# Kernel tuning notes

Hardware: AMD Instinct MI355X
Metric: run time of the kernel (lower is better)

## Reference

```python
import jax, jax.numpy as jnp
import numpy as np

# Kernel codes matching style 'L;O2;P2;Y2,1,1;R0.5;W1,1'
KERNEL_CODES = ['L', 'O', 'P', 'Y', 'R', 'W']
SM_TEMP = 1.0


def _norm_sq(q, k):
    # q: [n,l,h,e], k: [n,s,h,e] -> [n,h,l,s]
    q2 = jnp.einsum('nlhe,nlhe->nhl', q, q)[..., None]        # [n,h,l,1]
    k2 = jnp.einsum('nshe,nshe->nhs', k, k)[:, :, None, :]     # [n,h,1,s]
    qk = jnp.einsum('nlhe,nshe->nhls', q, k)
    return q2 + k2 - 2.0 * qk


def _kernel(code, q, k):
    if code == 'L':
        return jnp.einsum('nlhe,nshe->nhls', q, k)
    if code == 'O':  # -log(1 + ns^(p/2)), p=2
        return -jnp.log1p(_norm_sq(q, k))
    if code == 'P':  # -(ns)^(p/2), p=2
        return -_norm_sq(q, k)
    if code == 'Y':  # (alpha*<q,k> + c)^p, p=2, alpha=1, c=1
        d = jnp.einsum('nlhe,nshe->nhls', q, k)
        return (d + 1.0) ** 2
    if code == 'R':  # exp(-gamma*ns), gamma=0.5
        return jnp.exp(-0.5 * _norm_sq(q, k))
    if code == 'W':  # cos(ns/a)*exp(-ns/b), a=b=1
        ns = _norm_sq(q, k)
        return jnp.cos(ns) * jnp.exp(-ns)
    raise ValueError(code)


def setup_inputs() -> dict:
    key = jax.random.key(0)
    k1, k2, k3, k4 = jax.random.split(key, 4)
    N, L, S, H, E, K = 2, 1024, 1024, 8, 64, 6
    return {
        'query': jax.random.normal(k1, (N, L, H, E), dtype=jnp.float32),
        'key': jax.random.normal(k2, (N, S, H, E), dtype=jnp.float32),
        'attn_mask_add': jnp.zeros((N, L, S), dtype=jnp.float32),
        'key_lengths_add': jnp.zeros((N, S), dtype=jnp.float32),
        'M': jax.random.uniform(k3, (H, E, K), dtype=jnp.float32),
        'C': jax.random.uniform(k4, (K, H, E, E), dtype=jnp.float32),
    }


def reference(query, key, attn_mask_add, key_lengths_add, M, C):
    # mixture weights pi: [n,l,h,k]
    pi = jax.nn.softmax(jnp.einsum('nlhe,hek->nlhk', query, M), axis=-1)
    out = None
    for c, code in enumerate(KERNEL_CODES):
        # htilde = tanh(query @ C[c]): [n,l,h,e]
        htilde = jnp.tanh(jnp.einsum('nlhe,hef->nlhf', query, C[c]))
        qk = _kernel(code, htilde, key)                    # [n,h,l,s]
        qk = qk + attn_mask_add[:, None] + key_lengths_add[:, None, None, :]
        sm = jax.nn.softmax(SM_TEMP * qk, axis=-1)
        w = jnp.transpose(pi[..., c], (0, 2, 1))[..., None]  # [n,h,l,1]
        term = sm * w
        out = term if out is None else out + term
    return out
```

## Files before the change

kernel.cpp:

```cpp
#include <hip/hip_runtime.h>
#include <hip/hip_bf16.h>
#include <math.h>

#define N_  2
#define H_  8
#define G_  16
#define L_  1024
#define S_  1024
#define E_  64
#define NC_ 6

typedef __attribute__((ext_vector_type(4))) float floatx4;
typedef __attribute__((ext_vector_type(8))) short short8;

#define MFMA16 __builtin_amdgcn_mfma_f32_16x16x32_bf16

#define AHAT_OFF   0
#define AHAT_BYTES (NC_*G_*L_*128*2)
#define KHAT_OFF   (AHAT_OFF + AHAT_BYTES)
#define KHAT_BYTES (G_*S_*128*2)
#define PI_OFF     (KHAT_OFF + KHAT_BYTES)
#define PI_BYTES   (NC_*G_*L_*4)
#define HSQ_OFF    (PI_OFF + PI_BYTES)
#define HSQ_BYTES  (NC_*G_*L_*4)
#define KSQ_OFF    (HSQ_OFF + HSQ_BYTES)
#define KSQ_BYTES  (G_*S_*4)

__device__ __forceinline__ float ftanh(float x) {
  return 1.0f - 2.0f * __builtin_amdgcn_rcpf(__expf(2.0f*x) + 1.0f);
}

__global__ __launch_bounds__(256) void k_htilde(
    const float* __restrict__ q, const float* __restrict__ C,
    __hip_bfloat16* __restrict__ Ahat, float* __restrict__ hsq) {
  extern __shared__ char smraw[];
  float* qs = (float*)smraw;
  float* Cs = qs + 128*68;

  const int lch = blockIdx.x, c = blockIdx.y, g = blockIdx.z;
  const int n = g >> 3, h = g & 7;
  const int l0 = lch * 128;
  const int t = threadIdx.x;

  for (int u = t; u < 2048; u += 256) {
    int row = u >> 4, seg = u & 15;
    *(float4*)(qs + row*68 + seg*4) =
      *(const float4*)(q + (((size_t)(n*L_ + l0 + row))*H_ + h)*E_ + seg*4);
  }
  for (int u = t; u < 1024; u += 256) {
    int e = u >> 4, seg = u & 15;
    *(float4*)(Cs + e*68 + seg*4) =
      *(const float4*)(C + (((size_t)(c*8 + h))*64 + e)*64 + seg*4);
  }
  __syncthreads();

  const int rg = t >> 3, fg = t & 7;
  float acc[4][8];
  #pragma unroll
  for (int i = 0; i < 4; i++)
    #pragma unroll
    for (int j = 0; j < 8; j++) acc[i][j] = 0.0f;

  #pragma unroll 4
  for (int e0 = 0; e0 < 64; e0 += 4) {
    float4 q4[4];
    #pragma unroll
    for (int i = 0; i < 4; i++)
      q4[i] = *(const float4*)(qs + (rg*4 + i)*68 + e0);
    #pragma unroll
    for (int ee = 0; ee < 4; ee++) {
      float4 ca = *(const float4*)(Cs + (e0+ee)*68 + fg*8);
      float4 cb = *(const float4*)(Cs + (e0+ee)*68 + fg*8 + 4);
      float c8[8] = {ca.x, ca.y, ca.z, ca.w, cb.x, cb.y, cb.z, cb.w};
      #pragma unroll
      for (int i = 0; i < 4; i++) {
        float qv = (ee == 0) ? q4[i].x : (ee == 1) ? q4[i].y
                 : (ee == 2) ? q4[i].z : q4[i].w;
        #pragma unroll
        for (int j = 0; j < 8; j++) acc[i][j] = fmaf(qv, c8[j], acc[i][j]);
      }
    }
  }

  #pragma unroll
  for (int i = 0; i < 4; i++) {
    int l = l0 + rg*4 + i;
    size_t rowb = (((size_t)(c*G_ + g))*L_ + l) * 128;
    float ss = 0.0f;
    short8 hi8, lo8;
    #pragma unroll
    for (int j = 0; j < 8; j++) {
      float hv = ftanh(acc[i][j]);
      ss += hv*hv;
      __hip_bfloat16 hi = __float2bfloat16(hv);
      __hip_bfloat16 lo = __float2bfloat16(hv - __bfloat162float(hi));
      short hs, ls;
      __builtin_memcpy(&hs, &hi, 2);
      __builtin_memcpy(&ls, &lo, 2);
      hi8[j] = hs; lo8[j] = ls;
    }
    *(short8*)((char*)Ahat + (rowb + fg*8)*2)      = hi8;
    *(short8*)((char*)Ahat + (rowb + 64 + fg*8)*2) = lo8;
    ss += __shfl_xor(ss, 1); ss += __shfl_xor(ss, 2); ss += __shfl_xor(ss, 4);
    if (fg == 0) hsq[((size_t)(c*G_ + g))*L_ + l] = ss;
  }
}

__global__ __launch_bounds__(256) void k_pi(
    const float* __restrict__ q, const float* __restrict__ M,
    float* __restrict__ pi_t) {
  __shared__ float Ms[384];
  const int g = blockIdx.x >> 2, lch = blockIdx.x & 3;
  const int n = g >> 3, h = g & 7;
  const int t = threadIdx.x;
  const int l = lch*256 + t;
  for (int u = t; u < 384; u += 256) Ms[u] = M[h*384 + u];
  __syncthreads();
  const float* qrow = q + (((size_t)(n*L_ + l))*H_ + h)*E_;
  float p[6] = {0.f, 0.f, 0.f, 0.f, 0.f, 0.f};
  #pragma unroll 8
  for (int e = 0; e < 64; e++) {
    float qv = qrow[e];
    #pragma unroll
    for (int k = 0; k < 6; k++) p[k] = fmaf(qv, Ms[e*6 + k], p[k]);
  }
  float mx = p[0];
  #pragma unroll
  for (int k = 1; k < 6; k++) mx = fmaxf(mx, p[k]);
  float den = 0.f;
  #pragma unroll
  for (int k = 0; k < 6; k++) den += __expf(p[k] - mx);
  float rden = __builtin_amdgcn_rcpf(den);
  #pragma unroll
  for (int k = 0; k < 6; k++)
    pi_t[((size_t)(k*G_ + g))*L_ + l] = __expf(p[k] - mx) * rden;
}

__global__ __launch_bounds__(256) void k_key(
    const float* __restrict__ key, __hip_bfloat16* __restrict__ Khat,
    float* __restrict__ ksq) {
  int t = threadIdx.x; int wv = t >> 6; int lane = t & 63;
  int r = blockIdx.x*4 + wv;
  int g = r >> 10; int s = r & 1023; int n = g >> 3; int h = g & 7;
  float v = key[(((size_t)(n*S_ + s))*H_ + h)*E_ + lane];
  __hip_bfloat16 hi = __float2bfloat16(v);
  __hip_bfloat16 lo = __float2bfloat16(v - __bfloat162float(hi));
  size_t base = ((size_t)g*S_ + s)*128;
  Khat[base + lane]      = hi;
  Khat[base + 64 + lane] = lo;
  float sq = v*v;
  #pragma unroll
  for (int off = 32; off; off >>= 1) sq += __shfl_xor(sq, off);
  if (lane == 0) ksq[(size_t)g*S_ + s] = sq;
}

#define LDS_A6    0
#define LDS_ZRED  26112
#define LDS_MRED  27648
#define LDS_CST   29184
#define LDS_TOTAL 29952

__global__ __launch_bounds__(256, 2) void k_main(
    const __hip_bfloat16* __restrict__ Ahat, const __hip_bfloat16* __restrict__ Khat,
    const float* __restrict__ hsq, const float* __restrict__ ksq,
    const float* __restrict__ mask, const float* __restrict__ klen,
    const float* __restrict__ pi_t, float* __restrict__ out) {
  extern __shared__ char smraw[];
  char*   A6     = smraw + LDS_A6;
  float*  zred   = (float*)(smraw + LDS_ZRED);
  float*  mred   = (float*)(smraw + LDS_MRED);
  float2* cst    = (float2*)(smraw + LDS_CST);

  const int l0 = blockIdx.x * 16; const int g = blockIdx.y; const int n = g >> 3;
  const int t = threadIdx.x; const int w = t >> 6; const int lane = t & 63;
  const int quad = lane >> 4; const int lc = lane & 15;

  #pragma unroll
  for (int rep = 0; rep < 6; rep++) {
    int u = t + rep*256; int row = u >> 4, seg = u & 15;
    int cc = row >> 4, lr = row & 15;
    *(int4*)(A6 + row*272 + seg*16) =
      *(const int4*)((const char*)Ahat + (((size_t)(cc*G_ + g))*L_ + l0 + lr)*256 + seg*16);
  }
  __syncthreads();

  float h1p[4], nh2[4], h4h[4], nh5[4];
  #pragma unroll
  for (int i = 0; i < 4; i++) {
    int r = quad*4 + i;
    h1p[i] = 1.0f + hsq[((size_t)(1*G_ + g))*L_ + l0 + r];
    nh2[i] = 64.0f - hsq[((size_t)(2*G_ + g))*L_ + l0 + r];
    h4h[i] = -0.5f * hsq[((size_t)(4*G_ + g))*L_ + l0 + r];
    nh5[i] = -hsq[((size_t)(5*G_ + g))*L_ + l0 + r];
  }

  auto LOADB = [&](int st, short8 (&bf)[4]) {
    const char* base = (const char*)Khat +
        (((size_t)g)*S_ + st*64 + w*16 + lc)*256 + quad*16;
    #pragma unroll
    for (int kt = 0; kt < 4; kt++)
      bf[kt] = *(const short8*)(base + kt*64);
  };

  float Zc[4][4], zp[4], m3[4], z3[4];
  #pragma unroll
  for (int i = 0; i < 4; i++) {
    #pragma unroll
    for (int c = 0; c < 4; c++) Zc[c][i] = 0.0f;
    zp[i] = 0.0f; m3[i] = -INFINITY; z3[i] = 0.0f;
  }

  auto SWEEP1 = [&](int st, const short8 (&bf)[4]) {
    int scol = st*64 + w*16 + lc;
    float kq  = ksq[(size_t)g*S_ + scol];
    float klv = klen[(size_t)n*S_ + scol];
    float mv[4], Ev[4];
    #pragma unroll
    for (int i = 0; i < 4; i++) {
      mv[i] = mask[((size_t)(n*L_ + l0 + quad*4 + i))*S_ + scol] + klv;
      Ev[i] = __expf(mv[i]);
    }
    #pragma unroll
    for (int c = 0; c < 6; c++) {
      short8 af[4];
      #pragma unroll
      for (int kt = 0; kt < 4; kt++)
        af[kt] = *(const short8*)(A6 + (c*16 + lc)*272 + kt*64 + quad*16);
      floatx4 a = {0.f, 0.f, 0.f, 0.f};
      a = MFMA16(af[0], bf[0], a, 0,0,0);
      a = MFMA16(af[1], bf[1], a, 0,0,0);
      a = MFMA16(af[0], bf[2], a, 0,0,0);
      a = MFMA16(af[1], bf[3], a, 0,0,0);
      a = MFMA16(af[2], bf[0], a, 0,0,0);
      a = MFMA16(af[3], bf[1], a, 0,0,0);
      #pragma unroll
      for (int i = 0; i < 4; i++) {
        float d = a[i];
        if (c == 0) {
          Zc[0][i] = fmaf(Ev[i], __expf(d), Zc[0][i]);
        } else if (c == 1) {
          Zc[1][i] = fmaf(Ev[i],
              __builtin_amdgcn_rcpf(fmaf(-2.f, d, h1p[i] + kq)), Zc[1][i]);
        } else if (c == 2) {
          zp[i] += __expf(fmaf(2.f, d, nh2[i] - kq + mv[i]));
        } else if (c == 3) {
          float tt = d + 1.f;
          float x  = fmaf(tt, tt, mv[i]);
          float mn = fmaxf(m3[i], x);
          float e  = __expf(fminf(m3[i], x) - mn);
          z3[i] = (x > m3[i]) ? fmaf(z3[i], e, 1.0f) : (z3[i] + e);
          m3[i] = mn;
        } else if (c == 4) {
          Zc[2][i] = fmaf(Ev[i],
              __expf(__expf(d + fmaf(-0.5f, kq, h4h[i]))), Zc[2][i]);
        } else {
          float a5 = fmaf(2.f, d, nh5[i] - kq);
          Zc[3][i] = fmaf(Ev[i], __expf(__cosf(a5) * __expf(a5)), Zc[3][i]);
        }
      }
    }
  };

  {
    short8 bA[4], bB[4];
    LOADB(0, bA);
    #pragma unroll 1
    for (int st = 0; st < 16; st += 2) {
      LOADB(st + 1, bB);
      SWEEP1(st, bA);
      LOADB((st + 2) & 15, bA);
      SWEEP1(st + 1, bB);
    }
  }

  #pragma unroll
  for (int off = 1; off < 16; off <<= 1) {
    #pragma unroll
    for (int c = 0; c < 4; c++)
      #pragma unroll
      for (int i = 0; i < 4; i++) Zc[c][i] += __shfl_xor(Zc[c][i], off);
    #pragma unroll
    for (int i = 0; i < 4; i++) {
      zp[i] += __shfl_xor(zp[i], off);
      float mo = __shfl_xor(m3[i], off);
      float zo = __shfl_xor(z3[i], off);
      float mn = fmaxf(m3[i], mo);
      float e  = __expf(fminf(m3[i], mo) - mn);
      z3[i] = (mo > m3[i]) ? fmaf(z3[i], e, zo) : fmaf(zo, e, z3[i]);
      m3[i] = mn;
    }
  }
  if (lc == 0) {
    static const int cmap[4] = {0, 1, 4, 5};
    #pragma unroll
    for (int c = 0; c < 4; c++)
      #pragma unroll
      for (int i = 0; i < 4; i++) {
        zred[w*96 + cmap[c]*16 + quad*4 + i] = Zc[c][i];
        mred[w*96 + cmap[c]*16 + quad*4 + i] = 0.f;
      }
    #pragma unroll
    for (int i = 0; i < 4; i++) {
      zred[w*96 + 2*16 + quad*4 + i] = zp[i];
      mred[w*96 + 2*16 + quad*4 + i] = 0.f;
      zred[w*96 + 3*16 + quad*4 + i] = z3[i];
      mred[w*96 + 3*16 + quad*4 + i] = m3[i];
    }
  }
  __syncthreads();
  if (t < 96) {
    int c = t >> 4;
    float z = zred[t], m = mred[t];
    if (c == 3) {
      #pragma unroll
      for (int w2 = 1; w2 < 4; w2++) {
        float mo = mred[w2*96 + t], zo = zred[w2*96 + t];
        float mn = fmaxf(m, mo);
        float e  = __expf(fminf(m, mo) - mn);
        z = (mo > m) ? fmaf(z, e, zo) : fmaf(zo, e, z);
        m = mn;
      }
    } else {
      #pragma unroll
      for (int w2 = 1; w2 < 4; w2++) z += zred[w2*96 + t];
    }
    float piv = pi_t[((size_t)((t >> 4)*G_ + g))*L_ + l0 + (t & 15)];
    cst[t] = make_float2(piv / z, m);
  }
  __syncthreads();

  float ac[6][4], m3f[4];
  #pragma unroll
  for (int c = 0; c < 6; c++)
    #pragma unroll
    for (int i = 0; i < 4; i++) {
      float2 v = cst[c*16 + quad*4 + i];
      ac[c][i] = v.x;
      if (c == 3) m3f[i] = v.y;
    }

  auto SWEEP2 = [&](int st, const short8 (&bf)[4]) {
    int scol = st*64 + w*16 + lc;
    float kq  = ksq[(size_t)g*S_ + scol];
    float klv = klen[(size_t)n*S_ + scol];
    float mv[4], Ev[4];
    #pragma unroll
    for (int i = 0; i < 4; i++) {
      mv[i] = mask[((size_t)(n*L_ + l0 + quad*4 + i))*S_ + scol] + klv;
      Ev[i] = __expf(mv[i]);
    }
    float Sacc[4] = {0.f, 0.f, 0.f, 0.f};
    float Gg[4]   = {0.f, 0.f, 0.f, 0.f};
    #pragma unroll
    for (int c = 0; c < 6; c++) {
      short8 af[4];
      #pragma unroll
      for (int kt = 0; kt < 4; kt++)
        af[kt] = *(const short8*)(A6 + (c*16 + lc)*272 + kt*64 + quad*16);
      floatx4 a = {0.f, 0.f, 0.f, 0.f};
      a = MFMA16(af[0], bf[0], a, 0,0,0);
      a = MFMA16(af[1], bf[1], a, 0,0,0);
      a = MFMA16(af[0], bf[2], a, 0,0,0);
      a = MFMA16(af[1], bf[3], a, 0,0,0);
      a = MFMA16(af[2], bf[0], a, 0,0,0);
      a = MFMA16(af[3], bf[1], a, 0,0,0);
      #pragma unroll
      for (int i = 0; i < 4; i++) {
        float d = a[i];
        if (c == 0) {
          Sacc[i] = fmaf(ac[0][i], __expf(d), Sacc[i]);
        } else if (c == 1) {
          Sacc[i] = fmaf(ac[1][i],
              __builtin_amdgcn_rcpf(fmaf(-2.f, d, h1p[i] + kq)), Sacc[i]);
        } else if (c == 2) {
          Gg[i] = fmaf(ac[2][i], __expf(fmaf(2.f, d, nh2[i] - kq + mv[i])), Gg[i]);
        } else if (c == 3) {
          float tt = d + 1.f;
          float x  = fmaf(tt, tt, mv[i]);
          Gg[i] = fmaf(ac[3][i], __expf(x - m3f[i]), Gg[i]);
        } else if (c == 4) {
          Sacc[i] = fmaf(ac[4][i],
              __expf(__expf(d + fmaf(-0.5f, kq, h4h[i]))), Sacc[i]);
        } else {
          float a5 = fmaf(2.f, d, nh5[i] - kq);
          Sacc[i] = fmaf(ac[5][i], __expf(__cosf(a5) * __expf(a5)), Sacc[i]);
        }
      }
    }
    #pragma unroll
    for (int i = 0; i < 4; i++)
      out[(((size_t)g)*L_ + l0 + quad*4 + i)*S_ + scol] = fmaf(Ev[i], Sacc[i], Gg[i]);
  };

  {
    short8 bA[4], bB[4];
    LOADB(0, bA);
    #pragma unroll 1
    for (int st = 0; st < 16; st += 2) {
      LOADB(st + 1, bB);
      SWEEP2(st, bA);
      LOADB((st + 2) & 15, bA);
      SWEEP2(st + 1, bB);
    }
  }
}

extern "C" void kernel_launch(void* const* d_in, const int* in_sizes, int n_in,
                              void* d_out, int out_size, void* d_ws, size_t ws_size,
                              hipStream_t stream) {
  (void)in_sizes; (void)n_in; (void)out_size; (void)ws_size;
  const float* q    = (const float*)d_in[0];
  const float* key  = (const float*)d_in[1];
  const float* mask = (const float*)d_in[2];
  const float* klen = (const float*)d_in[3];
  const float* M    = (const float*)d_in[4];
  const float* C    = (const float*)d_in[5];
  char* ws = (char*)d_ws;
  __hip_bfloat16* Ahat = (__hip_bfloat16*)(ws + AHAT_OFF);
  __hip_bfloat16* Khat = (__hip_bfloat16*)(ws + KHAT_OFF);
  float* pi_t    = (float*)(ws + PI_OFF);
  float* hsq     = (float*)(ws + HSQ_OFF);
  float* ksq     = (float*)(ws + KSQ_OFF);
  float* out = (float*)d_out;

  k_htilde<<<dim3(8, 6, 16), 256, 52224, stream>>>(q, C, Ahat, hsq);
  k_key<<<4096, 256, 0, stream>>>(key, Khat, ksq);
  k_pi<<<64, 256, 0, stream>>>(q, M, pi_t);
  k_main<<<dim3(64, 16), 256, LDS_TOTAL, stream>>>(Ahat, Khat, hsq, ksq, mask, klen,
                                                   pi_t, out);
}
```

Baseline: 218.5 us.

## Swap MFMA operands so each lane owns one query row and writes float4 outputs

The MFMA operand order is swapped (K tile as A, query tile as B), which transposes the accumulator so each lane holds one query row and four consecutive key columns. Mask, key-length and ksq loads and the output store become float4 vector accesses, and per-row constants become scalars. The hi part of the query tile is held in registers while only the lo part stays in LDS, halving LDS size and per-sweep LDS reads. The row reduction now shuffles across quads instead of lanes. The cost is more live registers for the 12 cached A fragments, which could affect occupancy at the requested two blocks per SIMD.

```diff
diff --git a/kernel.cpp b/kernel.cpp
--- a/kernel.cpp
+++ b/kernel.cpp
@@ -154,11 +154,11 @@
   if (lane == 0) ksq[(size_t)g*S_ + s] = sq;
 }
 
-#define LDS_A6    0
-#define LDS_ZRED  26112
-#define LDS_MRED  27648
-#define LDS_CST   29184
-#define LDS_TOTAL 29952
+#define LDS_A6LO  0
+#define LDS_ZRED  13824
+#define LDS_MRED  15360
+#define LDS_CST   16896
+#define LDS_TOTAL 17664
 
 __global__ __launch_bounds__(256, 2) void k_main(
     const __hip_bfloat16* __restrict__ Ahat, const __hip_bfloat16* __restrict__ Khat,
@@ -166,7 +166,7 @@
     const float* __restrict__ mask, const float* __restrict__ klen,
     const float* __restrict__ pi_t, float* __restrict__ out) {
   extern __shared__ char smraw[];
-  char*   A6     = smraw + LDS_A6;
+  char*   A6     = smraw + LDS_A6LO;
   float*  zred   = (float*)(smraw + LDS_ZRED);
   float*  mred   = (float*)(smraw + LDS_MRED);
   float2* cst    = (float2*)(smraw + LDS_CST);
@@ -176,25 +176,30 @@
   const int quad = lane >> 4; const int lc = lane & 15;
 
   #pragma unroll
-  for (int rep = 0; rep < 6; rep++) {
-    int u = t + rep*256; int row = u >> 4, seg = u & 15;
+  for (int rep = 0; rep < 3; rep++) {
+    int u = t + rep*256; int row = u >> 3, seg = u & 7;
     int cc = row >> 4, lr = row & 15;
-    *(int4*)(A6 + row*272 + seg*16) =
-      *(const int4*)((const char*)Ahat + (((size_t)(cc*G_ + g))*L_ + l0 + lr)*256 + seg*16);
-  }
+    *(int4*)(A6 + row*144 + seg*16) =
+      *(const int4*)((const char*)Ahat +
+          (((size_t)(cc*G_ + g))*L_ + l0 + lr)*256 + 128 + seg*16);
+  }
+
+  short8 ah[6][2];
+  #pragma unroll
+  for (int cc = 0; cc < 6; cc++) {
+    const char* arow = (const char*)Ahat + (((size_t)(cc*G_ + g))*L_ + l0 + lc)*256;
+    ah[cc][0] = *(const short8*)(arow + quad*16);
+    ah[cc][1] = *(const short8*)(arow + 64 + quad*16);
+  }
+
+  float h1p = 1.0f  + hsq[((size_t)(1*G_ + g))*L_ + l0 + lc];
+  float nh2 = 64.0f - hsq[((size_t)(2*G_ + g))*L_ + l0 + lc];
+  float h4h = -0.5f * hsq[((size_t)(4*G_ + g))*L_ + l0 + lc];
+  float nh5 = -hsq[((size_t)(5*G_ + g))*L_ + l0 + lc];
+
   __syncthreads();
 
-  float h1p[4], nh2[4], h4h[4], nh5[4];
-  #pragma unroll
-  for (int i = 0; i < 4; i++) {
-    int r = quad*4 + i;
-    h1p[i] = 1.0f + hsq[((size_t)(1*G_ + g))*L_ + l0 + r];
-    nh2[i] = 64.0f - hsq[((size_t)(2*G_ + g))*L_ + l0 + r];
-    h4h[i] = -0.5f * hsq[((size_t)(4*G_ + g))*L_ + l0 + r];
-    nh5[i] = -hsq[((size_t)(5*G_ + g))*L_ + l0 + r];
-  }
-
-  auto LOADB = [&](int st, short8 (&bf)[4]) {
+  auto LOADK = [&](int st, short8 (&bf)[4]) {
     const char* base = (const char*)Khat +
         (((size_t)g)*S_ + st*64 + w*16 + lc)*256 + quad*16;
     #pragma unroll
@@ -202,60 +207,52 @@
       bf[kt] = *(const short8*)(base + kt*64);
   };
 
-  float Zc[4][4], zp[4], m3[4], z3[4];
-  #pragma unroll
-  for (int i = 0; i < 4; i++) {
-    #pragma unroll
-    for (int c = 0; c < 4; c++) Zc[c][i] = 0.0f;
-    zp[i] = 0.0f; m3[i] = -INFINITY; z3[i] = 0.0f;
-  }
+  float Zc0 = 0.f, Zc1 = 0.f, Zc2 = 0.f, Zc3 = 0.f, zp = 0.f;
+  float m3 = -INFINITY, z3 = 0.f;
 
   auto SWEEP1 = [&](int st, const short8 (&bf)[4]) {
-    int scol = st*64 + w*16 + lc;
-    float kq  = ksq[(size_t)g*S_ + scol];
-    float klv = klen[(size_t)n*S_ + scol];
+    int sb = st*64 + w*16 + quad*4;
+    float4 mk4 = *(const float4*)(mask + ((size_t)(n*L_ + l0 + lc))*S_ + sb);
+    float4 kl4 = *(const float4*)(klen + (size_t)n*S_ + sb);
+    float4 kq4 = *(const float4*)(ksq  + (size_t)g*S_ + sb);
+    float kq[4] = {kq4.x, kq4.y, kq4.z, kq4.w};
     float mv[4], Ev[4];
-    #pragma unroll
-    for (int i = 0; i < 4; i++) {
-      mv[i] = mask[((size_t)(n*L_ + l0 + quad*4 + i))*S_ + scol] + klv;
-      Ev[i] = __expf(mv[i]);
-    }
+    mv[0] = mk4.x + kl4.x; mv[1] = mk4.y + kl4.y;
+    mv[2] = mk4.z + kl4.z; mv[3] = mk4.w + kl4.w;
+    #pragma unroll
+    for (int i = 0; i < 4; i++) Ev[i] = __expf(mv[i]);
     #pragma unroll
     for (int c = 0; c < 6; c++) {
-      short8 af[4];
-      #pragma unroll
-      for (int kt = 0; kt < 4; kt++)
-        af[kt] = *(const short8*)(A6 + (c*16 + lc)*272 + kt*64 + quad*16);
+      short8 al0 = *(const short8*)(A6 + (c*16 + lc)*144 + quad*16);
+      short8 al1 = *(const short8*)(A6 + (c*16 + lc)*144 + 64 + quad*16);
       floatx4 a = {0.f, 0.f, 0.f, 0.f};
-      a = MFMA16(af[0], bf[0], a, 0,0,0);
-      a = MFMA16(af[1], bf[1], a, 0,0,0);
-      a = MFMA16(af[0], bf[2], a, 0,0,0);
-      a = MFMA16(af[1], bf[3], a, 0,0,0);
-      a = MFMA16(af[2], bf[0], a, 0,0,0);
-      a = MFMA16(af[3], bf[1], a, 0,0,0);
+      a = MFMA16(bf[0], ah[c][0], a, 0,0,0);
+      a = MFMA16(bf[1], ah[c][1], a, 0,0,0);
+      a = MFMA16(bf[0], al0,      a, 0,0,0);
+      a = MFMA16(bf[1], al1,      a, 0,0,0);
+      a = MFMA16(bf[2], ah[c][0], a, 0,0,0);
+      a = MFMA16(bf[3], ah[c][1], a, 0,0,0);
       #pragma unroll
       for (int i = 0; i < 4; i++) {
         float d = a[i];
         if (c == 0) {
-          Zc[0][i] = fmaf(Ev[i], __expf(d), Zc[0][i]);
+          Zc0 = fmaf(Ev[i], __expf(d), Zc0);
         } else if (c == 1) {
-          Zc[1][i] = fmaf(Ev[i],
-              __builtin_amdgcn_rcpf(fmaf(-2.f, d, h1p[i] + kq)), Zc[1][i]);
+          Zc1 = fmaf(Ev[i], __builtin_amdgcn_rcpf(fmaf(-2.f, d, h1p + kq[i])), Zc1);
         } else if (c == 2) {
-          zp[i] += __expf(fmaf(2.f, d, nh2[i] - kq + mv[i]));
+          zp += __expf(fmaf(2.f, d, nh2 - kq[i] + mv[i]));
         } else if (c == 3) {
           float tt = d + 1.f;
           float x  = fmaf(tt, tt, mv[i]);
-          float mn = fmaxf(m3[i], x);
-          float e  = __expf(fminf(m3[i], x) - mn);
-          z3[i] = (x > m3[i]) ? fmaf(z3[i], e, 1.0f) : (z3[i] + e);
-          m3[i] = mn;
+          float mn = fmaxf(m3, x);
+          float e  = __expf(fminf(m3, x) - mn);
+          z3 = (x > m3) ? fmaf(z3, e, 1.0f) : (z3 + e);
+          m3 = mn;
         } else if (c == 4) {
-          Zc[2][i] = fmaf(Ev[i],
-              __expf(__expf(d + fmaf(-0.5f, kq, h4h[i]))), Zc[2][i]);
+          Zc2 = fmaf(Ev[i], __expf(__expf(d + fmaf(-0.5f, kq[i], h4h))), Zc2);
         } else {
-          float a5 = fmaf(2.f, d, nh5[i] - kq);
-          Zc[3][i] = fmaf(Ev[i], __expf(__cosf(a5) * __expf(a5)), Zc[3][i]);
+          float a5 = fmaf(2.f, d, nh5 - kq[i]);
+          Zc3 = fmaf(Ev[i], __expf(__cosf(a5) * __expf(a5)), Zc3);
         }
       }
     }
@@ -263,49 +260,35 @@
 
   {
     short8 bA[4], bB[4];
-    LOADB(0, bA);
+    LOADK(0, bA);
     #pragma unroll 1
     for (int st = 0; st < 16; st += 2) {
-      LOADB(st + 1, bB);
+      LOADK(st + 1, bB);
       SWEEP1(st, bA);
-      LOADB((st + 2) & 15, bA);
+      LOADK((st + 2) & 15, bA);
       SWEEP1(st + 1, bB);
     }
   }
 
   #pragma unroll
-  for (int off = 1; off < 16; off <<= 1) {
-    #pragma unroll
-    for (int c = 0; c < 4; c++)
-      #pragma unroll
-      for (int i = 0; i < 4; i++) Zc[c][i] += __shfl_xor(Zc[c][i], off);
-    #pragma unroll
-    for (int i = 0; i < 4; i++) {
-      zp[i] += __shfl_xor(zp[i], off);
-      float mo = __shfl_xor(m3[i], off);
-      float zo = __shfl_xor(z3[i], off);
-      float mn = fmaxf(m3[i], mo);
-      float e  = __expf(fminf(m3[i], mo) - mn);
-      z3[i] = (mo > m3[i]) ? fmaf(z3[i], e, zo) : fmaf(zo, e, z3[i]);
-      m3[i] = mn;
-    }
-  }
-  if (lc == 0) {
-    static const int cmap[4] = {0, 1, 4, 5};
-    #pragma unroll
-    for (int c = 0; c < 4; c++)
-      #pragma unroll
-      for (int i = 0; i < 4; i++) {
-        zred[w*96 + cmap[c]*16 + quad*4 + i] = Zc[c][i];
-        mred[w*96 + cmap[c]*16 + quad*4 + i] = 0.f;
-      }
-    #pragma unroll
-    for (int i = 0; i < 4; i++) {
-      zred[w*96 + 2*16 + quad*4 + i] = zp[i];
-      mred[w*96 + 2*16 + quad*4 + i] = 0.f;
-      zred[w*96 + 3*16 + quad*4 + i] = z3[i];
-      mred[w*96 + 3*16 + quad*4 + i] = m3[i];
-    }
+  for (int off = 16; off < 64; off <<= 1) {
+    Zc0 += __shfl_xor(Zc0, off); Zc1 += __shfl_xor(Zc1, off);
+    Zc2 += __shfl_xor(Zc2, off); Zc3 += __shfl_xor(Zc3, off);
+    zp  += __shfl_xor(zp,  off);
+    float mo = __shfl_xor(m3, off);
+    float zo = __shfl_xor(z3, off);
+    float mn = fmaxf(m3, mo);
+    float e  = __expf(fminf(m3, mo) - mn);
+    z3 = (mo > m3) ? fmaf(z3, e, zo) : fmaf(zo, e, z3);
+    m3 = mn;
+  }
+  if (lane < 16) {
+    zred[w*96 + 0*16 + lc] = Zc0; mred[w*96 + 0*16 + lc] = 0.f;
+    zred[w*96 + 1*16 + lc] = Zc1; mred[w*96 + 1*16 + lc] = 0.f;
+    zred[w*96 + 2*16 + lc] = zp;  mred[w*96 + 2*16 + lc] = 0.f;
+    zred[w*96 + 3*16 + lc] = z3;  mred[w*96 + 3*16 + lc] = m3;
+    zred[w*96 + 4*16 + lc] = Zc2; mred[w*96 + 4*16 + lc] = 0.f;
+    zred[w*96 + 5*16 + lc] = Zc3; mred[w*96 + 5*16 + lc] = 0.f;
   }
   __syncthreads();
   if (t < 96) {
@@ -329,77 +312,71 @@
   }
   __syncthreads();
 
-  float ac[6][4], m3f[4];
-  #pragma unroll
-  for (int c = 0; c < 6; c++)
-    #pragma unroll
-    for (int i = 0; i < 4; i++) {
-      float2 v = cst[c*16 + quad*4 + i];
-      ac[c][i] = v.x;
-      if (c == 3) m3f[i] = v.y;
-    }
+  float ac0 = cst[0*16 + lc].x, ac1 = cst[1*16 + lc].x, ac2 = cst[2*16 + lc].x;
+  float ac3 = cst[3*16 + lc].x, ac4 = cst[4*16 + lc].x, ac5 = cst[5*16 + lc].x;
+  float m3f = cst[3*16 + lc].y;
 
   auto SWEEP2 = [&](int st, const short8 (&bf)[4]) {
-    int scol = st*64 + w*16 + lc;
-    float kq  = ksq[(size_t)g*S_ + scol];
-    float klv = klen[(size_t)n*S_ + scol];
+    int sb = st*64 + w*16 + quad*4;
+    float4 mk4 = *(const float4*)(mask + ((size_t)(n*L_ + l0 + lc))*S_ + sb);
+    float4 kl4 = *(const float4*)(klen + (size_t)n*S_ + sb);
+    float4 kq4 = *(const float4*)(ksq  + (size_t)g*S_ + sb);
+    float kq[4] = {kq4.x, kq4.y, kq4.z, kq4.w};
     float mv[4], Ev[4];
-    #pragma unroll
-    for (int i = 0; i < 4; i++) {
-      mv[i] = mask[((size_t)(n*L_ + l0 + quad*4 + i))*S_ + scol] + klv;
-      Ev[i] = __expf(mv[i]);
-    }
+    mv[0] = mk4.x + kl4.x; mv[1] = mk4.y + kl4.y;
+    mv[2] = mk4.z + kl4.z; mv[3] = mk4.w + kl4.w;
+    #pragma unroll
+    for (int i = 0; i < 4; i++) Ev[i] = __expf(mv[i]);
     float Sacc[4] = {0.f, 0.f, 0.f, 0.f};
     float Gg[4]   = {0.f, 0.f, 0.f, 0.f};
     #pragma unroll
     for (int c = 0; c < 6; c++) {
-      short8 af[4];
-      #pragma unroll
-      for (int kt = 0; kt < 4; kt++)
-        af[kt] = *(const short8*)(A6 + (c*16 + lc)*272 + kt*64 + quad*16);
+      short8 al0 = *(const short8*)(A6 + (c*16 + lc)*144 + quad*16);
+      short8 al1 = *(const short8*)(A6 + (c*16 + lc)*144 + 64 + quad*16);
       floatx4 a = {0.f, 0.f, 0.f, 0.f};
-      a = MFMA16(af[0], bf[0], a, 0,0,0);
-      a = MFMA16(af[1], bf[1], a, 0,0,0);
-      a = MFMA16(af[0], bf[2], a, 0,0,0);
-      a = MFMA16(af[1], bf[3], a, 0,0,0);
-      a = MFMA16(af[2], bf[0], a, 0,0,0);
-      a = MFMA16(af[3], bf[1], a, 0,0,0);
+      a = MFMA16(bf[0], ah[c][0], a, 0,0,0);
+      a = MFMA16(bf[1], ah[c][1], a, 0,0,0);
+      a = MFMA16(bf[0], al0,      a, 0,0,0);
+      a = MFMA16(bf[1], al1,      a, 0,0,0);
+      a = MFMA16(bf[2], ah[c][0], a, 0,0,0);
+      a = MFMA16(bf[3], ah[c][1], a, 0,0,0);
       #pragma unroll
       for (int i = 0; i < 4; i++) {
         float d = a[i];
         if (c == 0) {
-          Sacc[i] = fmaf(ac[0][i], __expf(d), Sacc[i]);
+          Sacc[i] = fmaf(ac0, __expf(d), Sacc[i]);
         } else if (c == 1) {
-          Sacc[i] = fmaf(ac[1][i],
-              __builtin_amdgcn_rcpf(fmaf(-2.f, d, h1p[i] + kq)), Sacc[i]);
+          Sacc[i] = fmaf(ac1, __builtin_amdgcn_rcpf(fmaf(-2.f, d, h1p + kq[i])), Sacc[i]);
         } else if (c == 2) {
-          Gg[i] = fmaf(ac[2][i], __expf(fmaf(2.f, d, nh2[i] - kq + mv[i])), Gg[i]);
+          Gg[i] = fmaf(ac2, __expf(fmaf(2.f, d, nh2 - kq[i] + mv[i])), Gg[i]);
         } else if (c == 3) {
           float tt = d + 1.f;
           float x  = fmaf(tt, tt, mv[i]);
-          Gg[i] = fmaf(ac[3][i], __expf(x - m3f[i]), Gg[i]);
+          Gg[i] = fmaf(ac3, __expf(x - m3f), Gg[i]);
         } else if (c == 4) {
-          Sacc[i] = fmaf(ac[4][i],
-              __expf(__expf(d + fmaf(-0.5f, kq, h4h[i]))), Sacc[i]);
+          Sacc[i] = fmaf(ac4, __expf(__expf(d + fmaf(-0.5f, kq[i], h4h))), Sacc[i]);
         } else {
-          float a5 = fmaf(2.f, d, nh5[i] - kq);
-          Sacc[i] = fmaf(ac[5][i], __expf(__cosf(a5) * __expf(a5)), Sacc[i]);
+          float a5 = fmaf(2.f, d, nh5 - kq[i]);
+          Sacc[i] = fmaf(ac5, __expf(__cosf(a5) * __expf(a5)), Sacc[i]);
         }
       }
     }
-    #pragma unroll
-    for (int i = 0; i < 4; i++)
-      out[(((size_t)g)*L_ + l0 + quad*4 + i)*S_ + scol] = fmaf(Ev[i], Sacc[i], Gg[i]);
+    float4 ov;
+    ov.x = fmaf(Ev[0], Sacc[0], Gg[0]);
+    ov.y = fmaf(Ev[1], Sacc[1], Gg[1]);
+    ov.z = fmaf(Ev[2], Sacc[2], Gg[2]);
+    ov.w = fmaf(Ev[3], Sacc[3], Gg[3]);
+    *(float4*)(out + (((size_t)g)*L_ + l0 + lc)*S_ + sb) = ov;
   };
 
   {
     short8 bA[4], bB[4];
-    LOADB(0, bA);
+    LOADK(0, bA);
     #pragma unroll 1
     for (int st = 0; st < 16; st += 2) {
-      LOADB(st + 1, bB);
+      LOADK(st + 1, bB);
       SWEEP2(st, bA);
-      LOADB((st + 2) & 15, bA);
+      LOADK((st + 2) & 15, bA);
       SWEEP2(st + 1, bB);
     }
   }
```

New measurement: 202.7 us. -7.2%, faster.
